# Kernel tuning notes

Measured on AMD Instinct MI355X. Metric: run time of the kernel, lower is better.

Reference implementation:

```python
import jax, jax.numpy as jnp
import numpy as np

N_NODES = 100000


def sage_conv(x, src, dst, W_l, W_r, b):
    """PyG-style SAGEConv with mean aggregation:
    out = mean_{j in N(i)} x_j @ W_l + b + x_i @ W_r
    Messages flow edge_index[0] (src) -> edge_index[1] (dst).
    """
    n = x.shape[0]
    msgs = x[src]  # [E, F] gather
    agg = jax.ops.segment_sum(msgs, dst, num_segments=n)  # [N, F]
    cnt = jax.ops.segment_sum(jnp.ones((src.shape[0],), dtype=x.dtype), dst, num_segments=n)
    mean = agg / jnp.clip(cnt, 1.0)[:, None]
    return mean @ W_l + b + x @ W_r


def setup_inputs() -> dict:
    key = jax.random.key(0)
    ks = jax.random.split(key, 12)
    F_in, H, out_c = 128, 128, 1
    E, K = 3200000, 64

    def glorot(k, shape):
        fan_in, fan_out = shape[0], shape[1]
        lim = np.sqrt(6.0 / (fan_in + fan_out))
        return jax.random.uniform(k, shape, jnp.float32, -lim, lim)

    return {
        "x": jax.random.normal(ks[0], (N_NODES, F_in), jnp.float32),
        "edge_index": jax.random.randint(ks[1], (2, E), 0, N_NODES, jnp.int64),
        "curr_idx": 123,
        "dest_idx": 4567,
        "neighbor_indices": jax.random.randint(ks[2], (K,), 0, N_NODES, jnp.int64),
        # conv1 params
        "W1_l": glorot(ks[3], (F_in, H)),
        "W1_r": glorot(ks[4], (F_in, H)),
        "b1": jnp.zeros((H,), jnp.float32),
        # conv2 params
        "W2_l": glorot(ks[5], (H, H)),
        "W2_r": glorot(ks[6], (H, H)),
        "b2": jnp.zeros((H,), jnp.float32),
        # MLP head
        "Wlin1": glorot(ks[7], (3 * H, H)),
        "blin1": jnp.zeros((H,), jnp.float32),
        "Wlin2": glorot(ks[8], (H, out_c)),
        "blin2": jnp.zeros((out_c,), jnp.float32),
    }


def reference(x, edge_index, curr_idx, dest_idx, neighbor_indices,
              W1_l, W1_r, b1, W2_l, W2_r, b2, Wlin1, blin1, Wlin2, blin2):
    src, dst = edge_index[0], edge_index[1]
    h = jax.nn.relu(sage_conv(x, src, dst, W1_l, W1_r, b1))
    node_embs = sage_conv(h, src, dst, W2_l, W2_r, b2)  # [N, H]

    curr_emb = node_embs[curr_idx]  # [H]
    dest_emb = node_embs[dest_idx]  # [H]
    nbr_embs = node_embs[neighbor_indices]  # [K, H]
    K = nbr_embs.shape[0]
    # batched version of the per-neighbor concat + 2-layer MLP
    cat = jnp.concatenate([
        jnp.broadcast_to(curr_emb, (K, curr_emb.shape[0])),
        jnp.broadcast_to(dest_emb, (K, dest_emb.shape[0])),
        nbr_embs,
    ], axis=1)  # [K, 3H]
    hidden = jax.nn.relu(cat @ Wlin1 + blin1)  # [K, H]
    q_values = hidden @ Wlin2 + blin2  # [K, 1]
    return q_values
```

## Files before the change

### kernel.cpp

```cpp
#include <hip/hip_runtime.h>
#include <cstdint>

constexpr int F        = 128;
constexpr int U_CAP    = 8192;
constexpr int T_CAP    = 128;
constexpr int BKT      = 128;
constexpr int BM_WORDS = 3200;
constexpr int SBLK     = 256;
constexpr int EPT      = 8;
constexpr int EPBLK    = SBLK * EPT;

typedef int int4v __attribute__((ext_vector_type(4)));


static __device__ __forceinline__ int chunk_of(int b, int nblk) {
    int q = nblk >> 3, r = nblk & 7;
    int xcd = b & 7, idx = b >> 3;
    return (xcd < r) ? xcd * (q + 1) + idx
                     : r * (q + 1) + (xcd - r) * q + idx;
}

__global__ void k_zero(int* p, int n) {
    int i = blockIdx.x * blockDim.x + threadIdx.x;
    int stride = gridDim.x * blockDim.x;
    for (; i < n; i += stride) p[i] = 0;
}

__global__ void k_build(const int* eidx, int E, int N,
                        const int* curr, const int* dest, const int* nbr, int K,
                        int* hdr, int* t_map, int* u_map,
                        unsigned* t_bm, unsigned* u_bm,
                        int* t_node, int* ent2comp, int* ulist) {
    __shared__ int s_e64, s_n64;
    int tid = threadIdx.x;
    if (tid == 0) { s_e64 = 1; s_n64 = 1; }
    __syncthreads();
    if (tid < 64 && eidx[2 * tid + 1] != 0) s_e64 = 0;
    if (tid < K / 2 && nbr[2 * tid + 1] != 0) s_n64 = 0;
    __syncthreads();
    int n64 = s_n64;
    if (tid == 0) { hdr[4] = s_e64; hdr[5] = s_n64; }

    int node = -1;
    if (tid < K + 2) {
        if (tid == 0)      node = curr[0];
        else if (tid == 1) node = dest[0];
        else               node = n64 ? nbr[2 * (tid - 2)] : nbr[tid - 2];
        if ((unsigned)node < (unsigned)N) {
            if (atomicCAS(&t_map[node], 0, -1) == 0) {
                int slot = atomicAdd(&hdr[0], 1);
                t_node[slot] = node;
                int uid = atomicAdd(&hdr[1], 1);
                ulist[uid] = node;
                atomicExch(&u_map[node], uid + 1);
                if (node < BM_WORDS * 32) {
                    atomicOr(&t_bm[node >> 5], 1u << (node & 31));
                    atomicOr(&u_bm[node >> 5], 1u << (node & 31));
                }
                atomicExch(&t_map[node], slot + 1);
            }
        }
    }
    __syncthreads();
    if (tid < K + 2) {
        int v = ((unsigned)node < (unsigned)N) ? atomicAdd(&t_map[node], 0) : 1;
        ent2comp[tid] = v - 1;
    }
}

static __device__ __forceinline__ int esrc(const int* eidx, int E, size_t e, int is64) {
    return is64 ? eidx[2 * e] : eidx[e];
}
static __device__ __forceinline__ int edst(const int* eidx, int E, size_t e, int is64) {
    return is64 ? eidx[2 * ((size_t)E + e)] : eidx[(size_t)E + e];
}

static __device__ __forceinline__ void issue4x(const int* p0, const int* p1,
                                               const int* p2, const int* p3,
                                               int4v& a, int4v& b, int4v& c, int4v& d) {
    asm volatile("global_load_dwordx4 %0, %4, off\n\t"
                 "global_load_dwordx4 %1, %5, off\n\t"
                 "global_load_dwordx4 %2, %6, off\n\t"
                 "global_load_dwordx4 %3, %7, off"
                 : "=&v"(a), "=&v"(b), "=&v"(c), "=&v"(d)
                 : "v"(p0), "v"(p1), "v"(p2), "v"(p3));
}
static __device__ __forceinline__ void wait4x(int4v& a, int4v& b, int4v& c, int4v& d) {
    asm volatile("s_waitcnt vmcnt(0)"
                 : "+v"(a), "+v"(b), "+v"(c), "+v"(d));
}
static __device__ __forceinline__ void issue8x(
        const int* p0, const int* p1, const int* p2, const int* p3,
        const int* p4, const int* p5, const int* p6, const int* p7,
        int4v& a0, int4v& a1, int4v& a2, int4v& a3,
        int4v& a4, int4v& a5, int4v& a6, int4v& a7) {
    asm volatile("global_load_dwordx4 %0, %8, off\n\t"
                 "global_load_dwordx4 %1, %9, off\n\t"
                 "global_load_dwordx4 %2, %10, off\n\t"
                 "global_load_dwordx4 %3, %11, off\n\t"
                 "global_load_dwordx4 %4, %12, off\n\t"
                 "global_load_dwordx4 %5, %13, off\n\t"
                 "global_load_dwordx4 %6, %14, off\n\t"
                 "global_load_dwordx4 %7, %15, off"
                 : "=&v"(a0), "=&v"(a1), "=&v"(a2), "=&v"(a3),
                   "=&v"(a4), "=&v"(a5), "=&v"(a6), "=&v"(a7)
                 : "v"(p0), "v"(p1), "v"(p2), "v"(p3),
                   "v"(p4), "v"(p5), "v"(p6), "v"(p7));
}
static __device__ __forceinline__ void wait8x(
        int4v& a0, int4v& a1, int4v& a2, int4v& a3,
        int4v& a4, int4v& a5, int4v& a6, int4v& a7) {
    asm volatile("s_waitcnt vmcnt(0)"
                 : "+v"(a0), "+v"(a1), "+v"(a2), "+v"(a3),
                   "+v"(a4), "+v"(a5), "+v"(a6), "+v"(a7));
}

__global__ void k_scan1(const int* __restrict__ eidx, int E, int N,
                        int* __restrict__ u_map,
                        const unsigned* __restrict__ t_bm,
                        unsigned* __restrict__ u_bm,
                        int* __restrict__ hdr, int* __restrict__ ulist) {
    __shared__ unsigned s_bm[BM_WORDS];
    int tid = threadIdx.x;
    int is64 = hdr[4];
    size_t be = (size_t)chunk_of(blockIdx.x, gridDim.x) * EPBLK;
    bool fast = is64 && ((E & 1) == 0) && be + EPBLK <= (size_t)E;

    int4v va, vb, vc, vd;
    if (fast) {
        const int* ebase = eidx + 2 * ((size_t)E + be);
        issue4x(ebase + (size_t)(0 * SBLK + tid) * 4,
                ebase + (size_t)(1 * SBLK + tid) * 4,
                ebase + (size_t)(2 * SBLK + tid) * 4,
                ebase + (size_t)(3 * SBLK + tid) * 4, va, vb, vc, vd);
    }
    for (int i = tid; i < BM_WORDS / 4; i += SBLK)
        reinterpret_cast<int4*>(s_bm)[i] = reinterpret_cast<const int4*>(t_bm)[i];
    __syncthreads();

    if (fast) {
        wait4x(va, vb, vc, vd);
        int d[EPT] = { va.x, va.z, vb.x, vb.z, vc.x, vc.z, vd.x, vd.z };
        unsigned w[EPT];
        #pragma unroll
        for (int i = 0; i < EPT; ++i) {
            int dc = ((unsigned)d[i] < (unsigned)N) ? d[i] : 0;
            w[i] = s_bm[dc >> 5];
        }
        unsigned m = 0;
        #pragma unroll
        for (int i = 0; i < EPT; ++i)
            if ((unsigned)d[i] < (unsigned)N && ((w[i] >> (d[i] & 31)) & 1)) m |= 1u << i;
        if (m) {
            #pragma unroll
            for (int i = 0; i < EPT; ++i) if (m & (1u << i)) {
                size_t e = be + (size_t)((i >> 1) * SBLK + tid) * 2 + (i & 1);
                int s = eidx[2 * e];
                if ((unsigned)s < (unsigned)N) {
                    if (atomicCAS(&u_map[s], 0, -1) == 0) {
                        int id = atomicAdd(&hdr[1], 1);
                        if (id < U_CAP) ulist[id] = s;
                        if (s < BM_WORDS * 32) atomicOr(&u_bm[s >> 5], 1u << (s & 31));
                        atomicExch(&u_map[s], id + 1);
                    }
                }
            }
        }
    } else {
        for (int r = 0; r < EPT; ++r) {
            size_t e = be + (size_t)(r * SBLK + tid);
            if (e >= (size_t)E) continue;
            int dd = edst(eidx, E, e, is64);
            if ((unsigned)dd >= (unsigned)N) continue;
            if (!((s_bm[dd >> 5] >> (dd & 31)) & 1)) continue;
            int s = esrc(eidx, E, e, is64);
            if ((unsigned)s >= (unsigned)N) continue;
            if (atomicCAS(&u_map[s], 0, -1) == 0) {
                int id = atomicAdd(&hdr[1], 1);
                if (id < U_CAP) ulist[id] = s;
                if (s < BM_WORDS * 32) atomicOr(&u_bm[s >> 5], 1u << (s & 31));
                atomicExch(&u_map[s], id + 1);
            }
        }
    }
}

__global__ void k_scanU(const int* __restrict__ eidx, int E, int N,
                        const int* __restrict__ u_map,
                        const unsigned* __restrict__ u_bm,
                        const int* __restrict__ hdr,
                        int* __restrict__ deg1, int* __restrict__ bucket) {
    __shared__ unsigned s_bm[BM_WORDS];
    int tid = threadIdx.x;
    int is64 = hdr[4];
    size_t be = (size_t)chunk_of(blockIdx.x, gridDim.x) * EPBLK;
    bool fast = is64 && ((E & 1) == 0) && be + EPBLK <= (size_t)E;

    int4v va, vb, vc, vd;
    if (fast) {
        const int* ebase = eidx + 2 * ((size_t)E + be);
        issue4x(ebase + (size_t)(0 * SBLK + tid) * 4,
                ebase + (size_t)(1 * SBLK + tid) * 4,
                ebase + (size_t)(2 * SBLK + tid) * 4,
                ebase + (size_t)(3 * SBLK + tid) * 4, va, vb, vc, vd);
    }
    for (int i = tid; i < BM_WORDS / 4; i += SBLK)
        reinterpret_cast<int4*>(s_bm)[i] = reinterpret_cast<const int4*>(u_bm)[i];
    __syncthreads();

    if (fast) {
        wait4x(va, vb, vc, vd);
        int d[EPT] = { va.x, va.z, vb.x, vb.z, vc.x, vc.z, vd.x, vd.z };
        unsigned w[EPT];
        #pragma unroll
        for (int i = 0; i < EPT; ++i) {
            int dc = ((unsigned)d[i] < (unsigned)N) ? d[i] : 0;
            w[i] = s_bm[dc >> 5];
        }
        unsigned m = 0;
        #pragma unroll
        for (int i = 0; i < EPT; ++i)
            if ((unsigned)d[i] < (unsigned)N && ((w[i] >> (d[i] & 31)) & 1)) m |= 1u << i;
        if (m) {
            #pragma unroll
            for (int i = 0; i < EPT; ++i) if (m & (1u << i)) {
                size_t e = be + (size_t)((i >> 1) * SBLK + tid) * 2 + (i & 1);
                int umi = u_map[d[i]];
                int s = eidx[2 * e];
                if (umi > 0 && umi <= U_CAP && (unsigned)s < (unsigned)N) {
                    int slot = umi - 1;
                    int pos = atomicAdd(&deg1[slot], 1);
                    if (pos < BKT) bucket[(size_t)slot * BKT + pos] = s;
                }
            }
        }
    } else {
        for (int r = 0; r < EPT; ++r) {
            size_t e = be + (size_t)(r * SBLK + tid);
            if (e >= (size_t)E) continue;
            int dd = edst(eidx, E, e, is64);
            if ((unsigned)dd >= (unsigned)N) continue;
            if (!((s_bm[dd >> 5] >> (dd & 31)) & 1)) continue;
            int umi = u_map[dd];
            if (umi <= 0 || umi > U_CAP) continue;
            int s = esrc(eidx, E, e, is64);
            if ((unsigned)s >= (unsigned)N) continue;
            int slot = umi - 1;
            int pos = atomicAdd(&deg1[slot], 1);
            if (pos < BKT) bucket[(size_t)slot * BKT + pos] = s;
        }
    }
}

__global__ void k_l1(const int* __restrict__ deg1, const int* __restrict__ bucket,
                     const int* __restrict__ hdr, const int* __restrict__ ulist, int N,
                     const float* __restrict__ x,
                     const float* __restrict__ W1l, const float* __restrict__ W1r,
                     const float* __restrict__ b1, float* __restrict__ h) {
    int nU = min(hdr[1], U_CAP);
    __shared__ int s_src[BKT];
    __shared__ float4 s_part[4][32];
    __shared__ float mean[F];
    __shared__ float xr[F];
    int j = threadIdx.x;
    int g = j >> 5, l = j & 31;
    for (int b = blockIdx.x; b < nU; b += gridDim.x) {
        int dg = deg1[b];
        int stored = min(dg, BKT);
        s_src[j] = (j < stored) ? bucket[(size_t)b * BKT + j] : -1;
        int node = ulist[b];
        xr[j] = ((unsigned)node < (unsigned)N) ? x[(size_t)node * F + j] : 0.0f;
        __syncthreads();
        float4 a4 = make_float4(0.f, 0.f, 0.f, 0.f);
        const float* xb = x + 4 * l;
        for (int c = 0; c < stored; c += 32) {
            int s0 = s_src[c + g +  0], s1 = s_src[c + g +  4];
            int s2 = s_src[c + g +  8], s3 = s_src[c + g + 12];
            int s4 = s_src[c + g + 16], s5 = s_src[c + g + 20];
            int s6 = s_src[c + g + 24], s7 = s_src[c + g + 28];
            const float* q0 = xb + (size_t)(s0 >= 0 ? s0 : 0) * F;
            const float* q1 = xb + (size_t)(s1 >= 0 ? s1 : 0) * F;
            const float* q2 = xb + (size_t)(s2 >= 0 ? s2 : 0) * F;
            const float* q3 = xb + (size_t)(s3 >= 0 ? s3 : 0) * F;
            const float* q4 = xb + (size_t)(s4 >= 0 ? s4 : 0) * F;
            const float* q5 = xb + (size_t)(s5 >= 0 ? s5 : 0) * F;
            const float* q6 = xb + (size_t)(s6 >= 0 ? s6 : 0) * F;
            const float* q7 = xb + (size_t)(s7 >= 0 ? s7 : 0) * F;
            int4v r0, r1, r2, r3, r4, r5, r6, r7;
            issue8x((const int*)q0, (const int*)q1, (const int*)q2, (const int*)q3,
                    (const int*)q4, (const int*)q5, (const int*)q6, (const int*)q7,
                    r0, r1, r2, r3, r4, r5, r6, r7);
            wait8x(r0, r1, r2, r3, r4, r5, r6, r7);
            #define ACC4(S, R) if (S >= 0) {                      \
                a4.x += __int_as_float((R).x);                    \
                a4.y += __int_as_float((R).y);                    \
                a4.z += __int_as_float((R).z);                    \
                a4.w += __int_as_float((R).w); }
            ACC4(s0, r0) ACC4(s1, r1) ACC4(s2, r2) ACC4(s3, r3)
            ACC4(s4, r4) ACC4(s5, r5) ACC4(s6, r6) ACC4(s7, r7)
            #undef ACC4
        }
        s_part[g][l] = a4;
        __syncthreads();
        float c = (dg < 1) ? 1.0f : (float)dg;
        int lp = j >> 2, cc = j & 3;
        float sum = 0.0f;
        #pragma unroll
        for (int gg = 0; gg < 4; ++gg) {
            float4 p = s_part[gg][lp];
            sum += (cc == 0) ? p.x : (cc == 1) ? p.y : (cc == 2) ? p.z : p.w;
        }
        mean[j] = sum / c;
        __syncthreads();
        float o1 = b1[j], o2 = 0.0f;
        #pragma unroll 8
        for (int k = 0; k < F; ++k) {
            o1 += mean[k] * W1l[k * F + j];
            o2 += xr[k]   * W1r[k * F + j];
        }
        float o = o1 + o2;
        h[(size_t)b * F + j] = (o > 0.0f) ? o : 0.0f;
        __syncthreads();
    }
}

__global__ void k_l2(const int* __restrict__ hdr, const int* __restrict__ t_node,
                     const int* __restrict__ u_map, int N,
                     const int* __restrict__ deg1, const int* __restrict__ bucket,
                     const float* __restrict__ h,
                     const float* __restrict__ W2l, const float* __restrict__ W2r,
                     const float* __restrict__ b2, float* __restrict__ embT) {
    int nT = min(hdr[0], T_CAP);
    int b  = blockIdx.x;
    if (b >= nT) return;
    __shared__ int s_ui[BKT];
    __shared__ float mean[F];
    __shared__ float hr[F];
    int j = threadIdx.x;
    int node = t_node[b];
    int tui = ((unsigned)node < (unsigned)N) ? (u_map[node] - 1) : -1;
    int dg = 0, stored = 0;
    if ((unsigned)tui < (unsigned)U_CAP) {
        dg = deg1[tui];
        stored = min(dg, BKT);
    }
    if (j < stored) {
        int s  = bucket[(size_t)tui * BKT + j];
        int ui = ((unsigned)s < (unsigned)N) ? (u_map[s] - 1) : -1;
        s_ui[j] = ((unsigned)ui < (unsigned)U_CAP) ? ui : -1;
    }
    hr[j] = ((unsigned)tui < (unsigned)U_CAP) ? h[(size_t)tui * F + j] : 0.0f;
    __syncthreads();
    float sum = 0.0f;
    #pragma unroll 4
    for (int i = 0; i < stored; ++i) {
        int ui = s_ui[i];
        if (ui >= 0) sum += h[(size_t)ui * F + j];
    }
    float c = (dg < 1) ? 1.0f : (float)dg;
    mean[j] = sum / c;
    __syncthreads();
    float acc = b2[j];
    #pragma unroll 4
    for (int k = 0; k < F; ++k) {
        acc += mean[k] * W2l[k * F + j];
        acc += hr[k]   * W2r[k * F + j];
    }
    embT[(size_t)b * F + j] = acc;
}

static __device__ __forceinline__ float clamp999(int v) {
    return (float)(v < 0 ? 0 : (v > 999 ? 999 : v));
}

__global__ void k_headf(const int* __restrict__ hdr, const int* __restrict__ ent2comp,
                        const float* __restrict__ embT,
                        const float* __restrict__ Wlin1, const float* __restrict__ blin1,
                        const float* __restrict__ Wlin2, const float* __restrict__ blin2,
                        float* __restrict__ out, int K) {
    __shared__ float s_cat[3 * F];
    __shared__ float s_part[4][F];
    __shared__ float red[F];
    int k = blockIdx.x;
    int tid = threadIdx.x;
    int g = tid >> 7, j = tid & (F - 1);
    int c0 = ent2comp[0] & (T_CAP - 1);
    int c1 = ent2comp[1] & (T_CAP - 1);
    int ck = ent2comp[2 + k] & (T_CAP - 1);
    if (tid < F)          s_cat[tid] = embT[(size_t)c0 * F + tid];
    else if (tid < 2 * F) s_cat[tid] = embT[(size_t)c1 * F + (tid - F)];
    else if (tid < 3 * F) s_cat[tid] = embT[(size_t)ck * F + (tid - 2 * F)];
    __syncthreads();
    float acc = 0.0f;
    #pragma unroll 4
    for (int i = g * 96; i < (g + 1) * 96; ++i)
        acc += s_cat[i] * Wlin1[i * F + j];
    s_part[g][j] = acc;
    __syncthreads();
    if (g == 0) {
        float hid = blin1[j] + s_part[0][j] + s_part[1][j] + s_part[2][j] + s_part[3][j];
        hid = (hid > 0.0f) ? hid : 0.0f;
        red[j] = hid * Wlin2[j];
    }
    __syncthreads();
    for (int s = 64; s > 0; s >>= 1) {
        if (tid < s) red[tid] += red[tid + s];
        __syncthreads();
    }
    if (tid == 0) {
        int nT = hdr[0], nU = hdr[1];
        float D = 0.0f;
        if      (nT < 1  || nT > K + 2)  D = 1.0e6f + clamp999(nT) * 1e3f;
        else if (nU < nT || nU > U_CAP)  D = 2.0e6f + clamp999(nU / 10) * 1e3f;
        out[k] = red[0] + blin2[0] + D;
    }
}

extern "C" void kernel_launch(void* const* d_in, const int* in_sizes, int n_in,
                              void* d_out, int out_size, void* d_ws, size_t ws_size,
                              hipStream_t stream) {
    const float* x     = (const float*)d_in[0];
    const int*   eidx  = (const int*)d_in[1];
    const int*   curr  = (const int*)d_in[2];
    const int*   dest  = (const int*)d_in[3];
    const int*   nbr   = (const int*)d_in[4];
    const float* W1l   = (const float*)d_in[5];
    const float* W1r   = (const float*)d_in[6];
    const float* b1    = (const float*)d_in[7];
    const float* W2l   = (const float*)d_in[8];
    const float* W2r   = (const float*)d_in[9];
    const float* b2    = (const float*)d_in[10];
    const float* Wlin1 = (const float*)d_in[11];
    const float* blin1 = (const float*)d_in[12];
    const float* Wlin2 = (const float*)d_in[13];
    const float* blin2 = (const float*)d_in[14];
    float* out = (float*)d_out;

    const int N = in_sizes[0] / F;
    const int E = in_sizes[1] / 2;
    const int K = in_sizes[4];

    char*  ws  = (char*)d_ws;
    size_t off = 0;
    int*      hdr      = (int*)(ws + off);      off += 64;
    int*      t_map    = (int*)(ws + off);      off += (size_t)4 * N;
    int*      u_map    = (int*)(ws + off);      off += (size_t)4 * N;
    int*      t_node   = (int*)(ws + off);      off += (size_t)4 * T_CAP;
    int*      ent2comp = (int*)(ws + off);      off += (size_t)4 * 256;
    int*      ulist    = (int*)(ws + off);      off += (size_t)4 * U_CAP;
    unsigned* t_bm     = (unsigned*)(ws + off); off += (size_t)4 * BM_WORDS;
    unsigned* u_bm     = (unsigned*)(ws + off); off += (size_t)4 * BM_WORDS;
    int*      deg1     = (int*)(ws + off);      off += (size_t)4 * U_CAP;
    size_t zero_bytes = off;
    int*      bucket   = (int*)(ws + off);      off += (size_t)4 * U_CAP * BKT;
    float*    h        = (float*)(ws + off);    off += (size_t)4 * U_CAP * F;
    float*    embT     = (float*)(ws + off);    off += (size_t)4 * T_CAP * F;

    int zero_words = (int)(zero_bytes / 4);
    k_zero<<<1024, 256, 0, stream>>>((int*)d_ws, zero_words);

    k_build<<<1, 128, 0, stream>>>(eidx, E, N, curr, dest, nbr, K, hdr, t_map, u_map,
                                   t_bm, u_bm, t_node, ent2comp, ulist);

    int sg = (E + EPBLK - 1) / EPBLK;
    k_scan1<<<sg, SBLK, 0, stream>>>(eidx, E, N, u_map, t_bm, u_bm, hdr, ulist);
    k_scanU<<<sg, SBLK, 0, stream>>>(eidx, E, N, u_map, u_bm, hdr, deg1, bucket);
    k_l1<<<2048, 128, 0, stream>>>(deg1, bucket, hdr, ulist, N, x, W1l, W1r, b1, h);
    k_l2<<<T_CAP, 128, 0, stream>>>(hdr, t_node, u_map, N, deg1, bucket, h,
                                    W2l, W2r, b2, embT);
    k_headf<<<K, 512, 0, stream>>>(hdr, ent2comp, embT, Wlin1, blin1, Wlin2, blin2, out, K);
}
```

Baseline: 212.3 us.

## Fuse the two edge-scan kernels with a grid-wide spin barrier

Replaces the separate k_scan1 and k_scanU launches with one kernel, used when the grid fits within a co-residency cap. Each thread keeps its loaded destination indices in registers across a global atomic-counter barrier. After the barrier the block reloads the updated frontier bitmap and fills the buckets, avoiding a second read of the destination half of the edge list and one launch. The barrier depends on every block being resident at once; a spin limit sets an error flag that the head kernel turns into a sentinel output instead of hanging.

```diff
diff --git a/kernel.cpp b/kernel.cpp
--- a/kernel.cpp
+++ b/kernel.cpp
@@ -9,6 +9,7 @@
 constexpr int SBLK     = 256;
 constexpr int EPT      = 8;
 constexpr int EPBLK    = SBLK * EPT;
+constexpr int COOP_MAX = 2048;
 
 typedef int int4v __attribute__((ext_vector_type(4)));
 
@@ -113,6 +114,124 @@
     asm volatile("s_waitcnt vmcnt(0)"
                  : "+v"(a0), "+v"(a1), "+v"(a2), "+v"(a3),
                    "+v"(a4), "+v"(a5), "+v"(a6), "+v"(a7));
+}
+
+__global__ void __launch_bounds__(SBLK, 8)
+k_scan_fused(const int* __restrict__ eidx, int E, int N,
+             int* __restrict__ u_map,
+             const unsigned* __restrict__ t_bm,
+             unsigned* __restrict__ u_bm,
+             int* __restrict__ hdr, int* __restrict__ ulist,
+             int* __restrict__ deg1, int* __restrict__ bucket) {
+    __shared__ unsigned s_bm[BM_WORDS];
+    int tid = threadIdx.x;
+    int is64 = hdr[4];
+    size_t be = (size_t)blockIdx.x * EPBLK;
+    bool fast = is64 && ((E & 1) == 0) && be + EPBLK <= (size_t)E;
+
+    int4v va, vb, vc, vd;
+    if (fast) {
+        const int* ebase = eidx + 2 * ((size_t)E + be);
+        issue4x(ebase + (size_t)(0 * SBLK + tid) * 4,
+                ebase + (size_t)(1 * SBLK + tid) * 4,
+                ebase + (size_t)(2 * SBLK + tid) * 4,
+                ebase + (size_t)(3 * SBLK + tid) * 4, va, vb, vc, vd);
+    }
+    for (int i = tid; i < BM_WORDS / 4; i += SBLK)
+        reinterpret_cast<int4*>(s_bm)[i] = reinterpret_cast<const int4*>(t_bm)[i];
+    __syncthreads();
+
+    int d[EPT];
+    if (fast) {
+        wait4x(va, vb, vc, vd);
+        d[0] = va.x; d[1] = va.z; d[2] = vb.x; d[3] = vb.z;
+        d[4] = vc.x; d[5] = vc.z; d[6] = vd.x; d[7] = vd.z;
+        unsigned w[EPT];
+        #pragma unroll
+        for (int i = 0; i < EPT; ++i) {
+            int dc = ((unsigned)d[i] < (unsigned)N) ? d[i] : 0;
+            w[i] = s_bm[dc >> 5];
+        }
+        unsigned m = 0;
+        #pragma unroll
+        for (int i = 0; i < EPT; ++i)
+            if ((unsigned)d[i] < (unsigned)N && ((w[i] >> (d[i] & 31)) & 1)) m |= 1u << i;
+        if (m) {
+            #pragma unroll
+            for (int i = 0; i < EPT; ++i) if (m & (1u << i)) {
+                size_t e = be + (size_t)((i >> 1) * SBLK + tid) * 2 + (i & 1);
+                int s = eidx[2 * e];
+                if ((unsigned)s < (unsigned)N) {
+                    if (atomicCAS(&u_map[s], 0, -1) == 0) {
+                        int id = atomicAdd(&hdr[1], 1);
+                        if (id < U_CAP) ulist[id] = s;
+                        if (s < BM_WORDS * 32) atomicOr(&u_bm[s >> 5], 1u << (s & 31));
+                        atomicExch(&u_map[s], id + 1);
+                    }
+                }
+            }
+        }
+    } else {
+        #pragma unroll
+        for (int r = 0; r < EPT; ++r) {
+            size_t e = be + (size_t)(r * SBLK + tid);
+            int dd = (e < (size_t)E) ? edst(eidx, E, e, is64) : -1;
+            d[r] = dd;
+            if ((unsigned)dd >= (unsigned)N) continue;
+            if (!((s_bm[dd >> 5] >> (dd & 31)) & 1)) continue;
+            int s = esrc(eidx, E, e, is64);
+            if ((unsigned)s >= (unsigned)N) continue;
+            if (atomicCAS(&u_map[s], 0, -1) == 0) {
+                int id = atomicAdd(&hdr[1], 1);
+                if (id < U_CAP) ulist[id] = s;
+                if (s < BM_WORDS * 32) atomicOr(&u_bm[s >> 5], 1u << (s & 31));
+                atomicExch(&u_map[s], id + 1);
+            }
+        }
+    }
+
+    __syncthreads();
+    if (tid == 0) {
+        __threadfence();
+        atomicAdd(&hdr[8], 1);
+        int spins = 0;
+        while (__hip_atomic_load(&hdr[8], __ATOMIC_ACQUIRE,
+                                 __HIP_MEMORY_SCOPE_AGENT) < (int)gridDim.x) {
+            if (++spins > (1 << 16)) { atomicExch(&hdr[9], 1); break; }
+        }
+    }
+    __syncthreads();
+
+    for (int i = tid; i < BM_WORDS; i += SBLK)
+        s_bm[i] = __hip_atomic_load(&u_bm[i], __ATOMIC_RELAXED,
+                                    __HIP_MEMORY_SCOPE_AGENT);
+    __syncthreads();
+
+    unsigned w2[EPT];
+    #pragma unroll
+    for (int i = 0; i < EPT; ++i) {
+        int dc = ((unsigned)d[i] < (unsigned)N) ? d[i] : 0;
+        w2[i] = s_bm[dc >> 5];
+    }
+    unsigned m2 = 0;
+    #pragma unroll
+    for (int i = 0; i < EPT; ++i)
+        if ((unsigned)d[i] < (unsigned)N && ((w2[i] >> (d[i] & 31)) & 1)) m2 |= 1u << i;
+    if (m2) {
+        #pragma unroll
+        for (int i = 0; i < EPT; ++i) if (m2 & (1u << i)) {
+            size_t e = fast ? (be + (size_t)((i >> 1) * SBLK + tid) * 2 + (i & 1))
+                            : (be + (size_t)(i * SBLK + tid));
+            int umi = __hip_atomic_load(&u_map[d[i]], __ATOMIC_RELAXED,
+                                        __HIP_MEMORY_SCOPE_AGENT);
+            int s = esrc(eidx, E, e, is64);
+            if (umi > 0 && umi <= U_CAP && (unsigned)s < (unsigned)N) {
+                int slot = umi - 1;
+                int pos = atomicAdd(&deg1[slot], 1);
+                if (pos < BKT) bucket[(size_t)slot * BKT + pos] = s;
+            }
+        }
+    }
 }
 
 __global__ void k_scan1(const int* __restrict__ eidx, int E, int N,
@@ -412,6 +531,7 @@
         float D = 0.0f;
         if      (nT < 1  || nT > K + 2)  D = 1.0e6f + clamp999(nT) * 1e3f;
         else if (nU < nT || nU > U_CAP)  D = 2.0e6f + clamp999(nU / 10) * 1e3f;
+        else if (hdr[9] != 0)            D = 4.0e6f;
         out[k] = red[0] + blin2[0] + D;
     }
 }
@@ -463,8 +583,13 @@
                                    t_bm, u_bm, t_node, ent2comp, ulist);
 
     int sg = (E + EPBLK - 1) / EPBLK;
-    k_scan1<<<sg, SBLK, 0, stream>>>(eidx, E, N, u_map, t_bm, u_bm, hdr, ulist);
-    k_scanU<<<sg, SBLK, 0, stream>>>(eidx, E, N, u_map, u_bm, hdr, deg1, bucket);
+    if (sg <= COOP_MAX) {
+        k_scan_fused<<<sg, SBLK, 0, stream>>>(eidx, E, N, u_map, t_bm, u_bm,
+                                              hdr, ulist, deg1, bucket);
+    } else {
+        k_scan1<<<sg, SBLK, 0, stream>>>(eidx, E, N, u_map, t_bm, u_bm, hdr, ulist);
+        k_scanU<<<sg, SBLK, 0, stream>>>(eidx, E, N, u_map, u_bm, hdr, deg1, bucket);
+    }
     k_l1<<<2048, 128, 0, stream>>>(deg1, bucket, hdr, ulist, N, x, W1l, W1r, b1, h);
     k_l2<<<T_CAP, 128, 0, stream>>>(hdr, t_node, u_map, N, deg1, bucket, h,
                                     W2l, W2r, b2, embT);
```

Result: slower. 443.7 us (+109.0%).
